# Kernel optimization log

Measured on AMD Instinct MI355X. Metric: run time of the kernel, lower is better.

## Reference

```python
import jax, jax.numpy as jnp
import numpy as np

N = 20000      # nodes
E = 640000     # edges (avg degree 32)
F = 128        # hidden_channels == num_filters
RBF = 64       # num_rbf
H = 8          # num_heads
DH = F // H    # head dim
T = 5          # number of distinct element types present in z
CUT = 5.0      # cutoff_upper (cutoff_lower = 0)


def setup_inputs() -> dict:
    key = jax.random.key(0)
    ks = jax.random.split(key, 20)
    s = 0.05
    inp = {
        "x": jax.random.normal(ks[0], (N, F), jnp.float32),
        "z": jax.random.randint(ks[1], (N,), 0, T, jnp.int32),
        "edge_index": jax.random.randint(ks[2], (2, E), 0, N, jnp.int32),
        "edge_weight": jax.random.uniform(ks[3], (E,), jnp.float32) * CUT,
        "edge_attr": jax.random.normal(ks[4], (E, RBF), jnp.float32),
        # ElemConv params
        "lin1_w": jax.random.normal(ks[5], (F, F), jnp.float32) / np.sqrt(F),
        "f_w1": jax.random.normal(ks[6], (F, RBF), jnp.float32) / np.sqrt(RBF),
        "f_b1": jnp.zeros((F,), jnp.float32),
        "f_w2": jax.random.normal(ks[7], (F, F), jnp.float32) / np.sqrt(F),
        "f_b2": jnp.zeros((F,), jnp.float32),
        # ElemAttn params
        "q_w": jax.random.normal(ks[8], (F, F), jnp.float32) / np.sqrt(F),
        "q_b": jax.random.normal(ks[9], (F,), jnp.float32) * s,
        "k_w": jax.random.normal(ks[10], (F, F), jnp.float32) / np.sqrt(F),
        "k_b": jax.random.normal(ks[11], (F,), jnp.float32) * s,
        "v_w": jax.random.normal(ks[12], (F, F), jnp.float32) / np.sqrt(F),
        "v_b": jax.random.normal(ks[13], (F,), jnp.float32) * s,
        "o1_w": jax.random.normal(ks[14], (F, F), jnp.float32) / np.sqrt(F),
        "o1_b": jax.random.normal(ks[15], (F,), jnp.float32) * s,
        "o2_w": jax.random.normal(ks[16], (F, F), jnp.float32) / np.sqrt(F),
        "o2_b": jax.random.normal(ks[17], (F,), jnp.float32) * s,
    }
    return inp


def reference(x, z, edge_index, edge_weight, edge_attr,
              lin1_w, f_w1, f_b1, f_w2, f_b2,
              q_w, q_b, k_w, k_b, v_w, v_b, o1_w, o1_b, o2_w, o2_b):
    silu = jax.nn.silu
    src, dst = edge_index[0], edge_index[1]

    # ---- ElemConv ----
    # CosineCutoff (cutoff_lower = 0)
    C = 0.5 * (jnp.cos(edge_weight * (jnp.pi / CUT)) + 1.0)
    C = C * (edge_weight < CUT).astype(x.dtype)
    # filter_net(edge_attr) * C
    W = silu(edge_attr @ f_w1.T + f_b1) @ f_w2.T + f_b2          # [E, F]
    W = W * C[:, None]
    xl = x @ lin1_w.T                                             # [N, F]
    msg = xl[src] * W                                             # [E, F]
    # aggregate by unique (z_j, dst) pair == dense [N, T] slot grid
    seg = dst * T + z[src]                                        # [E]
    y = jax.ops.segment_sum(msg, seg, num_segments=N * T).reshape(N, T, F)
    cnt = jax.ops.segment_sum(jnp.ones((E,), x.dtype), seg, num_segments=N * T)
    pm = (cnt > 0).astype(x.dtype).reshape(N, T)                  # presence mask

    # ---- ElemAttn (block-diagonal per target node over present slots) ----
    q = (y @ q_w.T + q_b).reshape(N, T, H, DH)
    k = (y @ k_w.T + k_b).reshape(N, T, H, DH)
    v = (y @ v_w.T + v_b).reshape(N, T, H, DH)
    attn = silu(jnp.einsum('nihd,njhd->nhij', q, k))              # [N, H, T, T]
    attn = attn * (pm[:, None, :, None] * pm[:, None, None, :])
    out = jnp.einsum('nhij,njhd->nihd', attn, v).reshape(N, T, F)
    out = out @ o1_w.T + o1_b                                     # [N, T, F]
    node = jnp.einsum('ntf,nt->nf', out, pm)                      # scatter-add by node
    return silu(node @ o2_w.T + o2_b)                             # [N, F]
```

## Files before the change

kernel.cpp:

```cpp
#include <hip/hip_runtime.h>

#define N_NODES 20000
#define E_EDGES 640000
#define F_DIM 128
#define RBF_DIM 64
#define T_TYPES 5
#define NSEG (N_NODES * T_TYPES)
#define EPB 128

typedef __attribute__((ext_vector_type(8))) short short8;
typedef __attribute__((ext_vector_type(4))) float f32x4;

__device__ __forceinline__ float silu_f(float x) { return x / (1.0f + __expf(-x)); }

__device__ __forceinline__ ushort f2bf(float f) {
  unsigned u = __float_as_uint(f);
  u += 0x7fffu + ((u >> 16) & 1u);
  return (ushort)(u >> 16);
}
__device__ __forceinline__ float bf2f(ushort u) {
  return __uint_as_float(((unsigned)u) << 16);
}
__device__ __forceinline__ unsigned cvt_pk(float lo, float hi) {
  unsigned r;
  asm("v_cvt_pk_bf16_f32 %0, %1, %2" : "=v"(r) : "v"(lo), "v"(hi));
  return r;
}
union S8U4 {
  short8 s;
  unsigned u[4];
};

__global__ __launch_bounds__(256) void prep_kernel(
    const float* __restrict__ w1, const float* __restrict__ w2,
    const float* __restrict__ qw, const float* __restrict__ kw,
    const float* __restrict__ vw, const float* __restrict__ o1w,
    const float* __restrict__ o2w, ushort* __restrict__ w1b,
    ushort* __restrict__ w2b, ushort* __restrict__ qwb,
    ushort* __restrict__ kwb, ushort* __restrict__ vwb,
    ushort* __restrict__ o1wb, ushort* __restrict__ o2wb) {
  int i = blockIdx.x * 256 + threadIdx.x;
  if (i < F_DIM * RBF_DIM) w1b[i] = f2bf(w1[i]);
  if (i < F_DIM * F_DIM) {
    w2b[i] = f2bf(w2[i]);
    qwb[i] = f2bf(qw[i]);
    kwb[i] = f2bf(kw[i]);
    vwb[i] = f2bf(vw[i]);
    o1wb[i] = f2bf(o1w[i]);
    o2wb[i] = f2bf(o2w[i]);
  }
}

__global__ __launch_bounds__(256) void hist_rank_kernel(
    const int* __restrict__ srcp, const int* __restrict__ dstp,
    const int* __restrict__ z, int* __restrict__ hist, int* __restrict__ rnk) {
  int e = blockIdx.x * 256 + threadIdx.x;
  int s = srcp[e];
  int seg = dstp[e] * T_TYPES + z[s];
  rnk[e] = atomicAdd(&hist[seg], 1);
}

__global__ __launch_bounds__(256) void scan1_kernel(const int* __restrict__ hist,
                                                    int* __restrict__ offs,
                                                    int* __restrict__ bsums) {
  __shared__ int lds[256];
  int tid = threadIdx.x;
  int base = blockIdx.x * 1024 + tid * 4;
  int v[4];
  int s = 0;
#pragma unroll
  for (int i = 0; i < 4; ++i) {
    v[i] = (base + i < NSEG) ? hist[base + i] : 0;
    s += v[i];
  }
  lds[tid] = s;
  __syncthreads();
  for (int d = 1; d < 256; d <<= 1) {
    int t = (tid >= d) ? lds[tid - d] : 0;
    __syncthreads();
    lds[tid] += t;
    __syncthreads();
  }
  int excl = lds[tid] - s;
#pragma unroll
  for (int i = 0; i < 4; ++i) {
    if (base + i < NSEG) offs[base + i] = excl;
    excl += v[i];
  }
  if (tid == 255) bsums[blockIdx.x] = lds[255];
}

__global__ __launch_bounds__(128) void scan2_kernel(int* __restrict__ bsums,
                                                    int nb) {
  __shared__ int lds[128];
  int tid = threadIdx.x;
  int v = (tid < nb) ? bsums[tid] : 0;
  lds[tid] = v;
  __syncthreads();
  for (int d = 1; d < 128; d <<= 1) {
    int t = (tid >= d) ? lds[tid - d] : 0;
    __syncthreads();
    lds[tid] += t;
    __syncthreads();
  }
  if (tid < nb) bsums[tid] = lds[tid] - v;
}

__global__ __launch_bounds__(256) void scan3_kernel(int* __restrict__ offs,
                                                    const int* __restrict__ bsums) {
  int tid = threadIdx.x;
  int base = blockIdx.x * 1024 + tid * 4;
  int add = bsums[blockIdx.x];
#pragma unroll
  for (int i = 0; i < 4; ++i)
    if (base + i < NSEG) offs[base + i] += add;
}

__global__ __launch_bounds__(256) void scatter_kernel(
    const int* __restrict__ srcp, const int* __restrict__ dstp,
    const int* __restrict__ z, const int* __restrict__ offs,
    const int* __restrict__ rnk, int* __restrict__ perm) {
  int e = blockIdx.x * 256 + threadIdx.x;
  int s = srcp[e];
  int seg = dstp[e] * T_TYPES + z[s];
  perm[offs[seg] + rnk[e]] = e;
}

__global__ __launch_bounds__(128) void lin1_kernel(const float* __restrict__ x,
                                                   const float* __restrict__ w,
                                                   ushort* __restrict__ xlb) {
  __shared__ float xs[8 * 128];
  int tid = threadIdx.x;
  int n0 = blockIdx.x * 8;
  const float4* xg = (const float4*)(x + (size_t)n0 * 128);
  float4* xs4 = (float4*)xs;
  for (int i = tid; i < 256; i += 128) xs4[i] = xg[i];
  __syncthreads();
  int f = tid;
  float acc[8] = {};
  const float4* w4 = (const float4*)(w + (size_t)f * 128);
  for (int j4 = 0; j4 < 32; ++j4) {
    float4 wv = w4[j4];
#pragma unroll
    for (int n = 0; n < 8; ++n) {
      float4 xv = xs4[n * 32 + j4];
      acc[n] += wv.x * xv.x + wv.y * xv.y + wv.z * xv.z + wv.w * xv.w;
    }
  }
  for (int n = 0; n < 8; ++n) xlb[(size_t)(n0 + n) * 128 + f] = f2bf(acc[n]);
}

__global__ __launch_bounds__(256, 4) void edge_mfma_kernel(
    const float* __restrict__ edge_attr, const int* __restrict__ srcp,
    const int* __restrict__ dstp, const float* __restrict__ ewp,
    const int* __restrict__ z, const int* __restrict__ perm,
    const ushort* __restrict__ w1b, const float* __restrict__ b1,
    const ushort* __restrict__ w2b, const float* __restrict__ b2,
    const ushort* __restrict__ xlb, float* __restrict__ y) {
  __shared__ ushort hs[128 * 136];
  __shared__ float sC[EPB];
  __shared__ int srcoff[EPB];
  __shared__ int sseg[EPB];
  __shared__ unsigned long long smask[2];

  const int tid = threadIdx.x;
  const int bid = (blockIdx.x & 7) * 625 + (blockIdx.x >> 3);
  const int e0 = bid * EPB;
  const int lane = tid & 63;
  const int w = tid >> 6;
  const int wm = w >> 1, wn = w & 1;
  const int lr = lane & 15, lh = lane >> 4;

  int prow[4];
#pragma unroll
  for (int fm = 0; fm < 4; ++fm) prow[fm] = perm[e0 + wm * 64 + fm * 16 + lr];

  float rb1[4], rb2[4];
#pragma unroll
  for (int fc = 0; fc < 4; ++fc) {
    int n = wn * 64 + fc * 16 + lr;
    rb1[fc] = b1[n];
    rb2[fc] = b2[n];
  }

  if (tid < EPB) {
    int e = perm[e0 + tid];
    int s = srcp[e];
    srcoff[tid] = s * 128;
    sseg[tid] = dstp[e] * T_TYPES + z[s];
    float wd = ewp[e];
    float c = 0.5f * (__cosf(wd * 0.6283185307179586f) + 1.0f);
    sC[tid] = (wd < 5.0f) ? c : 0.0f;
  }

  f32x4 acc[4][4] = {};
#pragma unroll
  for (int ks = 0; ks < 2; ++ks) {
    const int k0 = ks * 32;
    short8 af[4], bfr[4];
#pragma unroll
    for (int fm = 0; fm < 4; ++fm) {
      const float* ap = edge_attr + (size_t)prow[fm] * 64 + k0 + lh * 8;
      float4 a0 = *(const float4*)ap;
      float4 a1 = *(const float4*)(ap + 4);
      S8U4 t;
      t.u[0] = cvt_pk(a0.x, a0.y);
      t.u[1] = cvt_pk(a0.z, a0.w);
      t.u[2] = cvt_pk(a1.x, a1.y);
      t.u[3] = cvt_pk(a1.z, a1.w);
      af[fm] = t.s;
    }
#pragma unroll
    for (int fc = 0; fc < 4; ++fc)
      bfr[fc] = *(const short8*)(w1b + (size_t)(wn * 64 + fc * 16 + lr) * 64 +
                                 k0 + lh * 8);
#pragma unroll
    for (int fm = 0; fm < 4; ++fm)
#pragma unroll
      for (int fc = 0; fc < 4; ++fc)
        acc[fm][fc] = __builtin_amdgcn_mfma_f32_16x16x32_bf16(
            af[fm], bfr[fc], acc[fm][fc], 0, 0, 0);
  }

#pragma unroll
  for (int fm = 0; fm < 4; ++fm) {
#pragma unroll
    for (int fc = 0; fc < 4; ++fc) {
#pragma unroll
      for (int rp = 0; rp < 4; rp += 2) {
        int ml0 = wm * 64 + fm * 16 + lh * 4 + rp;
        int ml1 = ml0 + 1;
        int n = wn * 64 + fc * 16 + lr;
        float h0 = silu_f(acc[fm][fc][rp] + rb1[fc]);
        float h1 = silu_f(acc[fm][fc][rp + 1] + rb1[fc]);
        unsigned u = cvt_pk(h0, h1);
        hs[(ml0 * 256 + ((n * 2) ^ ((ml0 & 7) << 4))) >> 1] = (ushort)u;
        hs[(ml1 * 256 + ((n * 2) ^ ((ml1 & 7) << 4))) >> 1] = (ushort)(u >> 16);
      }
    }
  }
  __syncthreads();

  if (tid < EPB) {
    int head = (tid == 0) || (sseg[tid] != sseg[tid - 1]);
    unsigned long long m = __ballot(head);
    if ((tid & 63) == 0) smask[tid >> 6] = m;
  }

  f32x4 acc2[4][4] = {};
#pragma unroll
  for (int ks = 0; ks < 4; ++ks) {
    const int k0 = ks * 32;
    short8 af[4], bfr[4];
#pragma unroll
    for (int fm = 0; fm < 4; ++fm) {
      int ml = wm * 64 + fm * 16 + lr;
      int byte_in_row = (k0 * 2 + lh * 16) ^ ((ml & 7) << 4);
      af[fm] = *(const short8*)&hs[(ml * 256 + byte_in_row) >> 1];
    }
#pragma unroll
    for (int fc = 0; fc < 4; ++fc)
      bfr[fc] = *(const short8*)(w2b + (size_t)(wn * 64 + fc * 16 + lr) * 128 +
                                 k0 + lh * 8);
#pragma unroll
    for (int fm = 0; fm < 4; ++fm)
#pragma unroll
      for (int fc = 0; fc < 4; ++fc)
        acc2[fm][fc] = __builtin_amdgcn_mfma_f32_16x16x32_bf16(
            af[fm], bfr[fc], acc2[fm][fc], 0, 0, 0);
  }
  __syncthreads();

#pragma unroll
  for (int fm = 0; fm < 4; ++fm) {
#pragma unroll
    for (int rp = 0; rp < 4; rp += 2) {
      int ml0 = wm * 64 + fm * 16 + lh * 4 + rp;
      float c0 = sC[ml0], c1 = sC[ml0 + 1];
#pragma unroll
      for (int fc = 0; fc < 4; ++fc) {
        int n = wn * 64 + fc * 16 + lr;
        float v0 = (acc2[fm][fc][rp] + rb2[fc]) * c0;
        float v1 = (acc2[fm][fc][rp + 1] + rb2[fc]) * c1;
        *(unsigned*)&hs[n * 136 + ml0] = cvt_pk(v0, v1);
      }
    }
  }
  __syncthreads();

  {
    int cp = tid & 63;
    int q = tid >> 6;
    int rbase = q * 32;
    int c0 = cp * 2;
    unsigned mm = (unsigned)(smask[q >> 1] >> ((q & 1) * 32));
    float a0 = 0.0f, a1 = 0.0f;
    int cur = sseg[rbase];
    bool first = true;
#pragma unroll
    for (int it = 0; it < 4; ++it) {
      int r0 = rbase + it * 8;
      short8 m0 = *(const short8*)&hs[c0 * 136 + r0];
      short8 m1 = *(const short8*)&hs[(c0 + 1) * 136 + r0];
      unsigned xv[8];
#pragma unroll
      for (int j = 0; j < 8; ++j)
        xv[j] = *(const unsigned*)&xlb[(size_t)srcoff[r0 + j] + c0];
#pragma unroll
      for (int j = 0; j < 8; ++j) {
        int rr = it * 8 + j;
        if (rr && ((mm >> rr) & 1u)) {
          float* yp = &y[(size_t)cur * 128 + c0];
          if (first) {
            atomicAdd(yp, a0);
            atomicAdd(yp + 1, a1);
            first = false;
          } else {
            yp[0] = a0;
            yp[1] = a1;
          }
          a0 = a1 = 0.0f;
          cur = sseg[r0 + j];
        }
        a0 += bf2f((ushort)m0[j]) * bf2f((ushort)xv[j]);
        a1 += bf2f((ushort)m1[j]) * bf2f((ushort)(xv[j] >> 16));
      }
    }
    float* yp = &y[(size_t)cur * 128 + c0];
    atomicAdd(yp, a0);
    atomicAdd(yp + 1, a1);
  }
}

#define QS 136
#define NB 16
__global__ __launch_bounds__(256) void attn_out_kernel(
    const float* __restrict__ y, const int* __restrict__ hist,
    const ushort* __restrict__ qwb, const ushort* __restrict__ kwb,
    const ushort* __restrict__ vwb, const float* __restrict__ qb,
    const float* __restrict__ kb, const float* __restrict__ vb,
    const ushort* __restrict__ o1wb, const float* __restrict__ o1b,
    const ushort* __restrict__ o2wb, const float* __restrict__ o2b,
    float* __restrict__ outp) {
  __shared__ ushort bufA[80 * QS];
  __shared__ ushort bufB[80 * QS];
  __shared__ float aap[NB * 8 * 2 * 5];
  __shared__ float pmv[80];
  __shared__ float snpm[NB];
  __shared__ float sxb[3][128];

  const int tid = threadIdx.x;
  const int xcd = blockIdx.x & 7;
  const int loc = blockIdx.x >> 3;
  const int bid = (xcd < 2 ? xcd * 157 : 314 + (xcd - 2) * 156) + loc;
  const int n0 = bid * NB;
  const int row0 = n0 * T_TYPES;
  const int lane = tid & 63;
  const int w = tid >> 6;
  const int lr = lane & 15, lh = lane >> 4;

  if (tid < 128) {
    sxb[0][tid] = qb[tid];
    sxb[1][tid] = kb[tid];
    sxb[2][tid] = vb[tid];
  }
  if (tid < 80) pmv[tid] = (hist[(size_t)row0 + tid] > 0) ? 1.0f : 0.0f;

  short8 A[4][5];
#pragma unroll
  for (int ksi = 0; ksi < 4; ++ksi) {
#pragma unroll
    for (int fm = 0; fm < 5; ++fm) {
      const float* ap =
          y + (size_t)(row0 + fm * 16 + lr) * 128 + ksi * 32 + lh * 8;
      float4 a0 = *(const float4*)ap;
      float4 a1 = *(const float4*)(ap + 4);
      S8U4 t;
      t.u[0] = cvt_pk(a0.x, a0.y);
      t.u[1] = cvt_pk(a0.z, a0.w);
      t.u[2] = cvt_pk(a1.x, a1.y);
      t.u[3] = cvt_pk(a1.z, a1.w);
      A[ksi][fm] = t.s;
    }
  }
  __syncthreads();
  if (tid < NB) {
    float s = 0.0f;
#pragma unroll
    for (int t = 0; t < 5; ++t) s += pmv[tid * 5 + t];
    snpm[tid] = s;
  }

  auto do_proj = [&](const ushort* __restrict__ Wb, const float* bias_row,
                     ushort* __restrict__ dst) {
    f32x4 acc[5][2] = {};
#pragma unroll
    for (int ksi = 0; ksi < 4; ++ksi) {
      short8 B[2];
#pragma unroll
      for (int fc = 0; fc < 2; ++fc)
        B[fc] = *(const short8*)(Wb + (size_t)(w * 32 + fc * 16 + lr) * 128 +
                                 ksi * 32 + lh * 8);
#pragma unroll
      for (int fm = 0; fm < 5; ++fm)
#pragma unroll
        for (int fc = 0; fc < 2; ++fc)
          acc[fm][fc] = __builtin_amdgcn_mfma_f32_16x16x32_bf16(
              A[ksi][fm], B[fc], acc[fm][fc], 0, 0, 0);
    }
#pragma unroll
    for (int fm = 0; fm < 5; ++fm)
#pragma unroll
      for (int fc = 0; fc < 2; ++fc)
#pragma unroll
        for (int rp = 0; rp < 4; rp += 2) {
          int rrow = fm * 16 + lh * 4 + rp;
          int col = w * 32 + fc * 16 + lr;
          float v0 = acc[fm][fc][rp] + bias_row[col];
          float v1 = acc[fm][fc][rp + 1] + bias_row[col];
          unsigned u = cvt_pk(v0, v1);
          dst[rrow * QS + col] = (ushort)u;
          dst[(rrow + 1) * QS + col] = (ushort)(u >> 16);
        }
  };

  do_proj(qwb, sxb[0], bufA);
  do_proj(kwb, sxb[1], bufB);
  __syncthreads();

  {
    int n = tid >> 4, h = (tid >> 1) & 7, g = tid & 1;
    int i0 = g ? 3 : 0;
    int cnt = g ? 2 : 3;
    float kv[5][16];
#pragma unroll
    for (int j = 0; j < 5; ++j) {
      short8 v0 = *(const short8*)&bufB[(n * 5 + j) * QS + h * 16];
      short8 v1 = *(const short8*)&bufB[(n * 5 + j) * QS + h * 16 + 8];
#pragma unroll
      for (int d = 0; d < 8; ++d) {
        kv[j][d] = bf2f((ushort)v0[d]);
        kv[j][d + 8] = bf2f((ushort)v1[d]);
      }
    }
    float a[5] = {};
    for (int ii = 0; ii < cnt; ++ii) {
      int i = i0 + ii;
      float qv[16];
      short8 q0 = *(const short8*)&bufA[(n * 5 + i) * QS + h * 16];
      short8 q1 = *(const short8*)&bufA[(n * 5 + i) * QS + h * 16 + 8];
#pragma unroll
      for (int d = 0; d < 8; ++d) {
        qv[d] = bf2f((ushort)q0[d]);
        qv[d + 8] = bf2f((ushort)q1[d]);
      }
      float pmi = pmv[n * 5 + i];
#pragma unroll
      for (int j = 0; j < 5; ++j) {
        float dd = 0.0f;
#pragma unroll
        for (int d = 0; d < 16; ++d) dd += qv[d] * kv[j][d];
        a[j] += pmi * silu_f(dd);
      }
    }
#pragma unroll
    for (int j = 0; j < 5; ++j) aap[((n * 8 + h) * 2 + g) * 5 + j] = a[j];
  }
  __syncthreads();

  do_proj(vwb, sxb[2], bufA);
  __syncthreads();

  {
    int n = tid >> 4;
    int o = tid & 15;
    int f0 = o * 8;
    int h = f0 >> 4;
    float acc8[8] = {};
#pragma unroll
    for (int j = 0; j < 5; ++j) {
      float a = (aap[((n * 8 + h) * 2 + 0) * 5 + j] +
                 aap[((n * 8 + h) * 2 + 1) * 5 + j]) *
                pmv[n * 5 + j];
      short8 vv8 = *(const short8*)&bufA[(n * 5 + j) * QS + f0];
#pragma unroll
      for (int d = 0; d < 8; ++d) acc8[d] += a * bf2f((ushort)vv8[d]);
    }
    S8U4 t;
    t.u[0] = cvt_pk(acc8[0], acc8[1]);
    t.u[1] = cvt_pk(acc8[2], acc8[3]);
    t.u[2] = cvt_pk(acc8[4], acc8[5]);
    t.u[3] = cvt_pk(acc8[6], acc8[7]);
    *(short8*)&bufB[n * QS + f0] = t.s;
  }
  __syncthreads();

  {
    f32x4 acc[2] = {};
#pragma unroll
    for (int ksi = 0; ksi < 4; ++ksi) {
      short8 af = *(const short8*)&bufB[lr * QS + ksi * 32 + lh * 8];
      short8 B0 = *(const short8*)(o1wb + (size_t)(w * 32 + lr) * 128 +
                                   ksi * 32 + lh * 8);
      short8 B1 = *(const short8*)(o1wb + (size_t)(w * 32 + 16 + lr) * 128 +
                                   ksi * 32 + lh * 8);
      acc[0] = __builtin_amdgcn_mfma_f32_16x16x32_bf16(af, B0, acc[0], 0, 0, 0);
      acc[1] = __builtin_amdgcn_mfma_f32_16x16x32_bf16(af, B1, acc[1], 0, 0, 0);
    }
#pragma unroll
    for (int fc = 0; fc < 2; ++fc) {
      int col = w * 32 + fc * 16 + lr;
      float bb = o1b[col];
#pragma unroll
      for (int r = 0; r < 4; ++r) {
        int row = lh * 4 + r;
        bufA[row * QS + col] = f2bf(acc[fc][r] + snpm[row] * bb);
      }
    }
  }
  __syncthreads();

  {
    f32x4 acc[2] = {};
#pragma unroll
    for (int ksi = 0; ksi < 4; ++ksi) {
      short8 af = *(const short8*)&bufA[lr * QS + ksi * 32 + lh * 8];
      short8 B0 = *(const short8*)(o2wb + (size_t)(w * 32 + lr) * 128 +
                                   ksi * 32 + lh * 8);
      short8 B1 = *(const short8*)(o2wb + (size_t)(w * 32 + 16 + lr) * 128 +
                                   ksi * 32 + lh * 8);
      acc[0] = __builtin_amdgcn_mfma_f32_16x16x32_bf16(af, B0, acc[0], 0, 0, 0);
      acc[1] = __builtin_amdgcn_mfma_f32_16x16x32_bf16(af, B1, acc[1], 0, 0, 0);
    }
#pragma unroll
    for (int fc = 0; fc < 2; ++fc) {
      int col = w * 32 + fc * 16 + lr;
      float bb = o2b[col];
#pragma unroll
      for (int r = 0; r < 4; ++r) {
        int row = lh * 4 + r;
        outp[(size_t)(n0 + row) * 128 + col] = silu_f(acc[fc][r] + bb);
      }
    }
  }
}

extern "C" void kernel_launch(void* const* d_in, const int* in_sizes, int n_in,
                              void* d_out, int out_size, void* d_ws, size_t ws_size,
                              hipStream_t stream) {
  const float* x = (const float*)d_in[0];
  const int* z = (const int*)d_in[1];
  const int* ei = (const int*)d_in[2];
  const float* ew = (const float*)d_in[3];
  const float* ea = (const float*)d_in[4];
  const float* lin1_w = (const float*)d_in[5];
  const float* fw1 = (const float*)d_in[6];
  const float* fb1 = (const float*)d_in[7];
  const float* fw2 = (const float*)d_in[8];
  const float* fb2 = (const float*)d_in[9];
  const float* qw = (const float*)d_in[10];
  const float* qb = (const float*)d_in[11];
  const float* kw = (const float*)d_in[12];
  const float* kb = (const float*)d_in[13];
  const float* vw = (const float*)d_in[14];
  const float* vb = (const float*)d_in[15];
  const float* o1w = (const float*)d_in[16];
  const float* o1b = (const float*)d_in[17];
  const float* o2w = (const float*)d_in[18];
  const float* o2b = (const float*)d_in[19];
  float* outp = (float*)d_out;
  float* ws = (float*)d_ws;

  float* y = ws;
  ushort* xlb = (ushort*)(y + (size_t)NSEG * F_DIM);
  ushort* w1b = xlb + (size_t)N_NODES * F_DIM;
  ushort* w2b = w1b + F_DIM * RBF_DIM;
  ushort* qwb = w2b + F_DIM * F_DIM;
  ushort* kwb = qwb + F_DIM * F_DIM;
  ushort* vwb = kwb + F_DIM * F_DIM;
  ushort* o1wb = vwb + F_DIM * F_DIM;
  ushort* o2wb = o1wb + F_DIM * F_DIM;
  int* hist = (int*)(o2wb + F_DIM * F_DIM);
  int* offs = hist + NSEG;
  int* bsums = offs + NSEG;
  int* rnk = bsums + 128;
  int* perm = rnk + E_EDGES;

  const int* srcp = ei;
  const int* dstp = ei + E_EDGES;
  const int NB_SCAN = (NSEG + 1023) / 1024;

  hipMemsetAsync(y, 0, (size_t)NSEG * F_DIM * sizeof(float), stream);
  hipMemsetAsync(hist, 0, (size_t)NSEG * sizeof(int), stream);

  prep_kernel<<<64, 256, 0, stream>>>(fw1, fw2, qw, kw, vw, o1w, o2w, w1b, w2b,
                                      qwb, kwb, vwb, o1wb, o2wb);
  hist_rank_kernel<<<E_EDGES / 256, 256, 0, stream>>>(srcp, dstp, z, hist, rnk);
  scan1_kernel<<<NB_SCAN, 256, 0, stream>>>(hist, offs, bsums);
  scan2_kernel<<<1, 128, 0, stream>>>(bsums, NB_SCAN);
  scan3_kernel<<<NB_SCAN, 256, 0, stream>>>(offs, bsums);
  scatter_kernel<<<E_EDGES / 256, 256, 0, stream>>>(srcp, dstp, z, offs, rnk, perm);
  lin1_kernel<<<N_NODES / 8, 128, 0, stream>>>(x, lin1_w, xlb);
  edge_mfma_kernel<<<E_EDGES / EPB, 256, 0, stream>>>(ea, srcp, dstp, ew, z, perm,
                                                      w1b, fb1, w2b, fb2, xlb, y);
  attn_out_kernel<<<N_NODES / NB, 256, 0, stream>>>(y, hist, qwb, kwb, vwb, qb, kb,
                                                    vb, o1wb, o1b, o2wb, o2b, outp);
}
```

Baseline: 323.7 us.

## Use MFMA for lin1, fold scan3 into scatter, drop edge block swizzle

lin1 becomes a bf16 MFMA kernel: each block handles 80 nodes, x is converted to bf16 on the fly, and lin1_w is pre-converted to bf16 in prep. This replaces the fp32 scalar dot-product loop. The scan3 kernel is removed and scatter adds the per-block scan offset itself, saving one launch and one pass over offs. The edge kernel's block-index swizzle is also removed. These changes add bf16 rounding to lin1's inputs and may alter cache locality for the edge kernel.

```diff
diff --git a/kernel.cpp b/kernel.cpp
--- a/kernel.cpp
+++ b/kernel.cpp
@@ -35,10 +35,11 @@
     const float* __restrict__ w1, const float* __restrict__ w2,
     const float* __restrict__ qw, const float* __restrict__ kw,
     const float* __restrict__ vw, const float* __restrict__ o1w,
-    const float* __restrict__ o2w, ushort* __restrict__ w1b,
-    ushort* __restrict__ w2b, ushort* __restrict__ qwb,
-    ushort* __restrict__ kwb, ushort* __restrict__ vwb,
-    ushort* __restrict__ o1wb, ushort* __restrict__ o2wb) {
+    const float* __restrict__ o2w, const float* __restrict__ lw,
+    ushort* __restrict__ w1b, ushort* __restrict__ w2b,
+    ushort* __restrict__ qwb, ushort* __restrict__ kwb,
+    ushort* __restrict__ vwb, ushort* __restrict__ o1wb,
+    ushort* __restrict__ o2wb, ushort* __restrict__ lwb) {
   int i = blockIdx.x * 256 + threadIdx.x;
   if (i < F_DIM * RBF_DIM) w1b[i] = f2bf(w1[i]);
   if (i < F_DIM * F_DIM) {
@@ -48,6 +49,7 @@
     vwb[i] = f2bf(vw[i]);
     o1wb[i] = f2bf(o1w[i]);
     o2wb[i] = f2bf(o2w[i]);
+    lwb[i] = f2bf(lw[i]);
   }
 }
 
@@ -106,48 +108,63 @@
   if (tid < nb) bsums[tid] = lds[tid] - v;
 }
 
-__global__ __launch_bounds__(256) void scan3_kernel(int* __restrict__ offs,
-                                                    const int* __restrict__ bsums) {
-  int tid = threadIdx.x;
-  int base = blockIdx.x * 1024 + tid * 4;
-  int add = bsums[blockIdx.x];
-#pragma unroll
-  for (int i = 0; i < 4; ++i)
-    if (base + i < NSEG) offs[base + i] += add;
-}
-
 __global__ __launch_bounds__(256) void scatter_kernel(
     const int* __restrict__ srcp, const int* __restrict__ dstp,
     const int* __restrict__ z, const int* __restrict__ offs,
-    const int* __restrict__ rnk, int* __restrict__ perm) {
+    const int* __restrict__ bsums, const int* __restrict__ rnk,
+    int* __restrict__ perm) {
   int e = blockIdx.x * 256 + threadIdx.x;
   int s = srcp[e];
   int seg = dstp[e] * T_TYPES + z[s];
-  perm[offs[seg] + rnk[e]] = e;
-}
-
-__global__ __launch_bounds__(128) void lin1_kernel(const float* __restrict__ x,
-                                                   const float* __restrict__ w,
+  perm[offs[seg] + bsums[seg >> 10] + rnk[e]] = e;
+}
+
+__global__ __launch_bounds__(256) void lin1_kernel(const float* __restrict__ x,
+                                                   const ushort* __restrict__ lwb,
                                                    ushort* __restrict__ xlb) {
-  __shared__ float xs[8 * 128];
-  int tid = threadIdx.x;
-  int n0 = blockIdx.x * 8;
-  const float4* xg = (const float4*)(x + (size_t)n0 * 128);
-  float4* xs4 = (float4*)xs;
-  for (int i = tid; i < 256; i += 128) xs4[i] = xg[i];
-  __syncthreads();
-  int f = tid;
-  float acc[8] = {};
-  const float4* w4 = (const float4*)(w + (size_t)f * 128);
-  for (int j4 = 0; j4 < 32; ++j4) {
-    float4 wv = w4[j4];
-#pragma unroll
-    for (int n = 0; n < 8; ++n) {
-      float4 xv = xs4[n * 32 + j4];
-      acc[n] += wv.x * xv.x + wv.y * xv.y + wv.z * xv.z + wv.w * xv.w;
-    }
-  }
-  for (int n = 0; n < 8; ++n) xlb[(size_t)(n0 + n) * 128 + f] = f2bf(acc[n]);
+  const int tid = threadIdx.x;
+  const int lane = tid & 63;
+  const int w = tid >> 6;
+  const int lr = lane & 15, lh = lane >> 4;
+  const int r0 = blockIdx.x * 80;
+
+  f32x4 acc[5][2] = {};
+#pragma unroll
+  for (int ksi = 0; ksi < 4; ++ksi) {
+    short8 B[2];
+#pragma unroll
+    for (int fc = 0; fc < 2; ++fc)
+      B[fc] = *(const short8*)(lwb + (size_t)(w * 32 + fc * 16 + lr) * 128 +
+                               ksi * 32 + lh * 8);
+#pragma unroll
+    for (int fm = 0; fm < 5; ++fm) {
+      const float* ap =
+          x + (size_t)(r0 + fm * 16 + lr) * 128 + ksi * 32 + lh * 8;
+      float4 a0 = *(const float4*)ap;
+      float4 a1 = *(const float4*)(ap + 4);
+      S8U4 t;
+      t.u[0] = cvt_pk(a0.x, a0.y);
+      t.u[1] = cvt_pk(a0.z, a0.w);
+      t.u[2] = cvt_pk(a1.x, a1.y);
+      t.u[3] = cvt_pk(a1.z, a1.w);
+#pragma unroll
+      for (int fc = 0; fc < 2; ++fc)
+        acc[fm][fc] = __builtin_amdgcn_mfma_f32_16x16x32_bf16(
+            t.s, B[fc], acc[fm][fc], 0, 0, 0);
+    }
+  }
+#pragma unroll
+  for (int fm = 0; fm < 5; ++fm)
+#pragma unroll
+    for (int fc = 0; fc < 2; ++fc)
+#pragma unroll
+      for (int rp = 0; rp < 4; rp += 2) {
+        int rrow = fm * 16 + lh * 4 + rp;
+        int col = w * 32 + fc * 16 + lr;
+        unsigned u = cvt_pk(acc[fm][fc][rp], acc[fm][fc][rp + 1]);
+        xlb[(size_t)(r0 + rrow) * 128 + col] = (ushort)u;
+        xlb[(size_t)(r0 + rrow + 1) * 128 + col] = (ushort)(u >> 16);
+      }
 }
 
 __global__ __launch_bounds__(256, 4) void edge_mfma_kernel(
@@ -164,8 +181,7 @@
   __shared__ unsigned long long smask[2];
 
   const int tid = threadIdx.x;
-  const int bid = (blockIdx.x & 7) * 625 + (blockIdx.x >> 3);
-  const int e0 = bid * EPB;
+  const int e0 = blockIdx.x * EPB;
   const int lane = tid & 63;
   const int w = tid >> 6;
   const int wm = w >> 1, wn = w & 1;
@@ -580,7 +596,8 @@
   ushort* vwb = kwb + F_DIM * F_DIM;
   ushort* o1wb = vwb + F_DIM * F_DIM;
   ushort* o2wb = o1wb + F_DIM * F_DIM;
-  int* hist = (int*)(o2wb + F_DIM * F_DIM);
+  ushort* lwb = o2wb + F_DIM * F_DIM;
+  int* hist = (int*)(lwb + F_DIM * F_DIM);
   int* offs = hist + NSEG;
   int* bsums = offs + NSEG;
   int* rnk = bsums + 128;
@@ -593,14 +610,14 @@
   hipMemsetAsync(y, 0, (size_t)NSEG * F_DIM * sizeof(float), stream);
   hipMemsetAsync(hist, 0, (size_t)NSEG * sizeof(int), stream);
 
-  prep_kernel<<<64, 256, 0, stream>>>(fw1, fw2, qw, kw, vw, o1w, o2w, w1b, w2b,
-                                      qwb, kwb, vwb, o1wb, o2wb);
+  prep_kernel<<<64, 256, 0, stream>>>(fw1, fw2, qw, kw, vw, o1w, o2w, lin1_w,
+                                      w1b, w2b, qwb, kwb, vwb, o1wb, o2wb, lwb);
   hist_rank_kernel<<<E_EDGES / 256, 256, 0, stream>>>(srcp, dstp, z, hist, rnk);
   scan1_kernel<<<NB_SCAN, 256, 0, stream>>>(hist, offs, bsums);
   scan2_kernel<<<1, 128, 0, stream>>>(bsums, NB_SCAN);
-  scan3_kernel<<<NB_SCAN, 256, 0, stream>>>(offs, bsums);
-  scatter_kernel<<<E_EDGES / 256, 256, 0, stream>>>(srcp, dstp, z, offs, rnk, perm);
-  lin1_kernel<<<N_NODES / 8, 128, 0, stream>>>(x, lin1_w, xlb);
+  scatter_kernel<<<E_EDGES / 256, 256, 0, stream>>>(srcp, dstp, z, offs, bsums,
+                                                    rnk, perm);
+  lin1_kernel<<<N_NODES / 80, 256, 0, stream>>>(x, lwb, xlb);
   edge_mfma_kernel<<<E_EDGES / EPB, 256, 0, stream>>>(ea, srcp, dstp, ew, z, perm,
                                                       w1b, fb1, w2b, fb2, xlb, y);
   attn_out_kernel<<<N_NODES / NB, 256, 0, stream>>>(y, hist, qwb, kwb, vwb, qb, kb,
```

Result: faster. 303.5 us (-6.2%).
